# Kernel tuning notes

Measured on AMD Instinct MI355X. Metric: run time of the kernel, lower is better.

## Reference

```python
import jax, jax.numpy as jnp
import numpy as np

DIM = 1024
HEADS = 16
HEAD_DIM = DIM // HEADS
SCALE = HEAD_DIM ** -0.5


def setup_inputs() -> dict:
    key = jax.random.key(0)
    k1, k2, k3, k4 = jax.random.split(key, 4)
    x = jax.random.normal(k1, (2, 2048, DIM), dtype=jnp.float32)
    # nn.Linear(dim, 3*dim, bias=False): weight shape (3*dim, dim), y = x @ W.T
    w_qkv = jax.random.normal(k2, (3 * DIM, DIM), dtype=jnp.float32) * (DIM ** -0.5)
    w_proj = jax.random.normal(k3, (DIM, DIM), dtype=jnp.float32) * (DIM ** -0.5)
    head_w = jnp.ones((HEADS,), dtype=jnp.float32)
    return {"x": x, "w_qkv": w_qkv, "w_proj": w_proj, "head_w": head_w}


def reference(x, w_qkv, w_proj, head_w) -> jnp.ndarray:
    B, N, C = x.shape
    qkv = jnp.einsum("bnc,dc->bnd", x, w_qkv)  # [B,N,3C]
    qkv = qkv.reshape(B, N, 3, HEADS, HEAD_DIM).transpose(2, 0, 3, 1, 4)
    q, k, v = qkv[0], qkv[1], qkv[2]  # each [B,H,N,Dh]
    attn = jnp.einsum("bhqd,bhkd->bhqk", q, k) * SCALE  # [B,H,N,N]
    attn = jax.nn.softmax(attn, axis=-1)
    out = jnp.einsum("bhqk,bhkd->bhqd", attn, v)  # [B,H,N,Dh]
    hw = jax.nn.softmax(head_w)[None, :, None, None]
    out = out * hw
    out = out.transpose(0, 2, 1, 3).reshape(B, N, C)
    return jnp.einsum("bnc,dc->bnd", out, w_proj)
```

## Files before the change

### kernel.cpp

```cpp
#include <hip/hip_runtime.h>

typedef _Float16 half_t;
typedef _Float16 half8 __attribute__((ext_vector_type(8)));
typedef _Float16 half4_t __attribute__((ext_vector_type(4)));
typedef _Float16 half2_t __attribute__((ext_vector_type(2)));
typedef float floatx4 __attribute__((ext_vector_type(4)));
typedef float floatx16 __attribute__((ext_vector_type(16)));
typedef unsigned int uint4v __attribute__((ext_vector_type(4)));

#define B_SZ 2
#define SEQ 2048
#define DIM_ 1024
#define NH 16
#define DH 64
#define ROWS (B_SZ * SEQ)
#define NJS 2

__device__ __forceinline__ void gl2lds16(const void* g, void* l) {
  __builtin_amdgcn_global_load_lds((const __attribute__((address_space(1))) unsigned int*)g,
                                   (__attribute__((address_space(3))) unsigned int*)l, 16, 0, 0);
}

__device__ __forceinline__ float fexp2(float x) {
#if __has_builtin(__builtin_amdgcn_exp2f)
  return __builtin_amdgcn_exp2f(x);
#else
  return __expf(x * 0.6931471805599453f);
#endif
}

__device__ __forceinline__ unsigned cvtpk_u32(float a, float b) {
#if __has_builtin(__builtin_amdgcn_cvt_pkrtz)
  return __builtin_bit_cast(unsigned, __builtin_amdgcn_cvt_pkrtz(a, b));
#else
  half2_t h; h.x = (half_t)a; h.y = (half_t)b;
  return __builtin_bit_cast(unsigned, h);
#endif
}

__device__ __forceinline__ half8 pack8(float p0, float p1, float p2, float p3,
                                       float p4, float p5, float p6, float p7) {
  uint4v u;
  u.x = cvtpk_u32(p0, p1);
  u.y = cvtpk_u32(p2, p3);
  u.z = cvtpk_u32(p4, p5);
  u.w = cvtpk_u32(p6, p7);
  return __builtin_bit_cast(half8, u);
}

__global__ __launch_bounds__(256) void convert_all(const float4* __restrict__ x,
                                                   const float4* __restrict__ wq,
                                                   const float4* __restrict__ wp,
                                                   half4_t* __restrict__ dst,
                                                   int nx, int nq, int np) {
  int i = blockIdx.x * blockDim.x + threadIdx.x;
  float4 v;
  if (i < nx) v = x[i];
  else if (i < nx + nq) v = wq[i - nx];
  else if (i < nx + nq + np) v = wp[i - nx - nq];
  else return;
  half4_t h;
  h.x = (half_t)v.x; h.y = (half_t)v.y; h.z = (half_t)v.z; h.w = (half_t)v.w;
  dst[i] = h;
}

template <int MODE, int BN>
__global__ __launch_bounds__(256) void gemm32(const half_t* __restrict__ A,
                                              const half_t* __restrict__ Bt,
                                              half_t* __restrict__ q16,
                                              half_t* __restrict__ k16,
                                              half_t* __restrict__ vT16,
                                              float* __restrict__ outp) {
  constexpr int K = 1024;
  constexpr int NT = BN / 64;
  __shared__ __align__(16) half_t a_lds[128 * 64];
  __shared__ __align__(16) half_t b_lds[BN * 64];
  const int t = threadIdx.x;
  const int wave = t >> 6, lane = t & 63;
  const int l31 = lane & 31, hw = lane >> 5;
  const int wm = wave >> 1, wn = wave & 1;
  const int row0 = blockIdx.y * 128, col0 = blockIdx.x * BN;

  floatx16 acc[2][NT];
#pragma unroll
  for (int i = 0; i < 2; ++i)
#pragma unroll
    for (int j = 0; j < NT; ++j)
#pragma unroll
      for (int r = 0; r < 16; ++r) acc[i][j][r] = 0.f;

  for (int k0 = 0; k0 < K; k0 += 64) {
#pragma unroll
    for (int hi = 0; hi < 4; ++hi) {
      int s = t + hi * 256;
      int row = s >> 3, c = s & 7;
      int sc = c ^ (row & 7);
      gl2lds16(A + (size_t)(row0 + row) * K + (k0 + sc * 8), a_lds + (wave * 64 + hi * 256) * 8);
    }
#pragma unroll
    for (int hi = 0; hi < BN / 32; ++hi) {
      int s = t + hi * 256;
      int row = s >> 3, c = s & 7;
      int sc = c ^ (row & 7);
      gl2lds16(Bt + (size_t)(col0 + row) * K + (k0 + sc * 8), b_lds + (wave * 64 + hi * 256) * 8);
    }
    __syncthreads();
    half8 af[2][4], bf[NT][4];
#pragma unroll
    for (int mt = 0; mt < 2; ++mt) {
      int row = wm * 64 + mt * 32 + l31;
#pragma unroll
      for (int kf = 0; kf < 4; ++kf)
        af[mt][kf] = *(const half8*)(a_lds + row * 64 + ((kf * 2 + hw) ^ (row & 7)) * 8);
    }
#pragma unroll
    for (int nt = 0; nt < NT; ++nt) {
      int row = wn * (BN / 2) + nt * 32 + l31;
#pragma unroll
      for (int kf = 0; kf < 4; ++kf)
        bf[nt][kf] = *(const half8*)(b_lds + row * 64 + ((kf * 2 + hw) ^ (row & 7)) * 8);
    }
#pragma unroll
    for (int kf = 0; kf < 4; ++kf)
#pragma unroll
      for (int mt = 0; mt < 2; ++mt)
#pragma unroll
        for (int nt = 0; nt < NT; ++nt)
          acc[mt][nt] =
              __builtin_amdgcn_mfma_f32_32x32x16_f16(af[mt][kf], bf[nt][kf], acc[mt][nt], 0, 0, 0);
    __syncthreads();
  }

  if (MODE == 0) {
    const int which = col0 >> 10;
#pragma unroll
    for (int mt = 0; mt < 2; ++mt)
#pragma unroll
      for (int nt = 0; nt < NT; ++nt) {
        int growb = row0 + wm * 64 + mt * 32;
        int gcol = col0 + wn * (BN / 2) + nt * 32 + l31;
        int hc = gcol & 1023, h = hc >> 6, d = hc & 63;
        if (which == 2) {
#pragma unroll
          for (int rq = 0; rq < 4; ++rq) {
            int grow = growb + 8 * rq + 4 * hw;
            int b = grow >> 11, n0 = grow & 2047;
            int bh = b * NH + h;
            half4_t h4;
            h4.x = (half_t)acc[mt][nt][rq * 4 + 0];
            h4.y = (half_t)acc[mt][nt][rq * 4 + 1];
            h4.z = (half_t)acc[mt][nt][rq * 4 + 2];
            h4.w = (half_t)acc[mt][nt][rq * 4 + 3];
            *(half4_t*)(vT16 + ((size_t)bh * DH + d) * SEQ + n0) = h4;
          }
        } else {
#pragma unroll
          for (int r = 0; r < 16; ++r) {
            int grow = growb + (r & 3) + 8 * (r >> 2) + 4 * hw;
            int b = grow >> 11, n = grow & 2047;
            int bh = b * NH + h;
            float v = acc[mt][nt][r];
            if (which == 0)
              q16[((size_t)bh * SEQ + n) * DH + d] =
                  (half_t)(v * 0.1803368801111204f);
            else
              k16[((size_t)bh * SEQ + n) * DH + d] = (half_t)v;
          }
        }
      }
  } else {
#pragma unroll
    for (int mt = 0; mt < 2; ++mt)
#pragma unroll
      for (int nt = 0; nt < NT; ++nt) {
        int growb = row0 + wm * 64 + mt * 32;
        int gcol = col0 + wn * (BN / 2) + nt * 32 + l31;
#pragma unroll
        for (int r = 0; r < 16; ++r) {
          int grow = growb + (r & 3) + 8 * (r >> 2) + 4 * hw;
          outp[(size_t)grow * DIM_ + gcol] = acc[mt][nt][r];
        }
      }
  }
}

__global__ __launch_bounds__(256, 3) void attn_p1(const half_t* __restrict__ q16,
                                                  const half_t* __restrict__ k16,
                                                  const half_t* __restrict__ vT16,
                                                  half_t* __restrict__ opart,
                                                  float* __restrict__ psums) {
  __shared__ __align__(16) half_t k_lds[2][64 * 64];
  __shared__ __align__(16) half_t v_lds[2][64 * 64];

  const int t = threadIdx.x;
  const int wave = t >> 6, lane = t & 63;
  const int l31 = lane & 31, hw = lane >> 5;
  const int blk = blockIdx.x;
  const int js = blk & (NJS - 1), qt = (blk >> 1) & 15, bh = blk >> 5;
  const half_t* qp = q16 + (size_t)bh * SEQ * DH;
  const half_t* kp = k16 + (size_t)bh * SEQ * DH;
  const half_t* vp = vT16 + (size_t)bh * DH * SEQ;
  const int q0w = qt * 128 + wave * 32;
  const int jbase = js * (SEQ / NJS);
  constexpr int NJT = (SEQ / NJS) / 64;

  const int s0 = t, s1 = t + 256;
  const int r0_ = s0 >> 3, c0_ = (s0 & 7) ^ (r0_ & 7);
  const int r1_ = s1 >> 3, c1_ = (s1 & 7) ^ (r1_ & 7);

  half8 qf[4];
#pragma unroll
  for (int kf = 0; kf < 4; ++kf)
    qf[kf] = *(const half8*)(qp + (size_t)(q0w + l31) * DH + kf * 16 + hw * 8);

  floatx16 o[2];
#pragma unroll
  for (int i = 0; i < 2; ++i)
#pragma unroll
    for (int r = 0; r < 16; ++r) o[i][r] = 0.f;
  float psum = 0.f;

  gl2lds16(kp + (size_t)(jbase + r0_) * DH + c0_ * 8, &k_lds[0][(wave * 64) * 8]);
  gl2lds16(vp + (size_t)r0_ * SEQ + jbase + c0_ * 8, &v_lds[0][(wave * 64) * 8]);
  gl2lds16(kp + (size_t)(jbase + r1_) * DH + c1_ * 8, &k_lds[0][(wave * 64 + 256) * 8]);
  gl2lds16(vp + (size_t)r1_ * SEQ + jbase + c1_ * 8, &v_lds[0][(wave * 64 + 256) * 8]);

  int cur = 0;
  for (int jt = 0; jt < NJT; ++jt) {
    __syncthreads();

    if (jt + 1 < NJT) {
      const int j0 = jbase + (jt + 1) * 64, nb = cur ^ 1;
      gl2lds16(kp + (size_t)(j0 + r0_) * DH + c0_ * 8, &k_lds[nb][(wave * 64) * 8]);
      gl2lds16(vp + (size_t)r0_ * SEQ + j0 + c0_ * 8, &v_lds[nb][(wave * 64) * 8]);
      gl2lds16(kp + (size_t)(j0 + r1_) * DH + c1_ * 8, &k_lds[nb][(wave * 64 + 256) * 8]);
      gl2lds16(vp + (size_t)r1_ * SEQ + j0 + c1_ * 8, &v_lds[nb][(wave * 64 + 256) * 8]);
    }

    const half_t* kl = k_lds[cur];
    const half_t* vl = v_lds[cur];

    floatx16 st[2];
#pragma unroll
    for (int m = 0; m < 2; ++m)
#pragma unroll
      for (int r = 0; r < 16; ++r) st[m][r] = 0.f;
    __builtin_amdgcn_s_setprio(1);
#pragma unroll
    for (int kf = 0; kf < 4; ++kf)
#pragma unroll
      for (int m = 0; m < 2; ++m) {
        int row = m * 32 + l31;
        half8 kb = *(const half8*)(kl + row * 64 + ((kf * 2 + hw) ^ (row & 7)) * 8);
        st[m] = __builtin_amdgcn_mfma_f32_32x32x16_f16(kb, qf[kf], st[m], 0, 0, 0);
      }
    __builtin_amdgcn_s_setprio(0);

    half8 pa[2][2];
#pragma unroll
    for (int m = 0; m < 2; ++m) {
      float p[16];
#pragma unroll
      for (int r = 0; r < 16; ++r) p[r] = fexp2(st[m][r]);
      float a0 = (p[0] + p[1]) + (p[2] + p[3]);
      float a1 = (p[4] + p[5]) + (p[6] + p[7]);
      float a2 = (p[8] + p[9]) + (p[10] + p[11]);
      float a3 = (p[12] + p[13]) + (p[14] + p[15]);
      psum += (a0 + a1) + (a2 + a3);
      pa[m][0] = pack8(p[0], p[1], p[2], p[3], p[4], p[5], p[6], p[7]);
      pa[m][1] = pack8(p[8], p[9], p[10], p[11], p[12], p[13], p[14], p[15]);
    }

    __builtin_amdgcn_s_setprio(1);
#pragma unroll
    for (int s = 0; s < 4; ++s) {
#pragma unroll
      for (int dt = 0; dt < 2; ++dt) {
        int row = dt * 32 + l31;
        int ca = ((s * 2 + 0) ^ (row & 7));
        int cb = ((s * 2 + 1) ^ (row & 7));
        half4_t va = *(const half4_t*)(vl + row * 64 + ca * 8 + hw * 4);
        half4_t vb = *(const half4_t*)(vl + row * 64 + cb * 8 + hw * 4);
        half8 v8 = __builtin_shufflevector(va, vb, 0, 1, 2, 3, 4, 5, 6, 7);
        o[dt] = __builtin_amdgcn_mfma_f32_32x32x16_f16(pa[s >> 1][s & 1], v8, o[dt], 0, 0, 0);
      }
    }
    __builtin_amdgcn_s_setprio(0);
    cur ^= 1;
  }

  psum += __shfl_xor(psum, 32, 64);
  if (hw == 0) psums[((size_t)(js * 32 + bh)) * SEQ + q0w + l31] = psum;

#pragma unroll
  for (int dt = 0; dt < 2; ++dt)
#pragma unroll
    for (int r = 0; r < 16; ++r) {
      int n = q0w + (r & 3) + 8 * (r >> 2) + 4 * hw;
      opart[((size_t)(js * 32 + bh) * SEQ + n) * DH + dt * 32 + l31] = (half_t)o[dt][r];
    }
}

__global__ __launch_bounds__(256) void combine(const half_t* __restrict__ opart,
                                               const float* __restrict__ psums,
                                               const float* __restrict__ head_w,
                                               half_t* __restrict__ attn16) {
  int idx = blockIdx.x * blockDim.x + threadIdx.x;
  int d4 = idx & 15, n = (idx >> 4) & 2047, bh = idx >> 15;
  int h = bh & 15, b = bh >> 4;
  const size_t jstr = (size_t)32 * SEQ * DH;
  size_t off = ((size_t)bh * SEQ + n) * DH + d4 * 4;

  float sx = 0.f, sy = 0.f, sz = 0.f, sw2 = 0.f, ps = 0.f;
#pragma unroll
  for (int js = 0; js < NJS; ++js) {
    half4_t ov = *(const half4_t*)(opart + js * jstr + off);
    sx += (float)ov.x; sy += (float)ov.y; sz += (float)ov.z; sw2 += (float)ov.w;
    ps += psums[(size_t)js * 32 * SEQ + (size_t)bh * SEQ + n];
  }

  float mw = head_w[0];
#pragma unroll
  for (int i = 1; i < NH; ++i) mw = fmaxf(mw, head_w[i]);
  float sw = 0.f;
#pragma unroll
  for (int i = 0; i < NH; ++i) sw += __expf(head_w[i] - mw);
  float hwv = __expf(head_w[h] - mw) / sw;

  float scl = hwv / ps;
  half4_t r;
  r.x = (half_t)(sx * scl);
  r.y = (half_t)(sy * scl);
  r.z = (half_t)(sz * scl);
  r.w = (half_t)(sw2 * scl);
  *(half4_t*)(attn16 + ((size_t)(b * SEQ + n)) * DIM_ + h * DH + d4 * 4) = r;
}

extern "C" void kernel_launch(void* const* d_in, const int* in_sizes, int n_in,
                              void* d_out, int out_size, void* d_ws, size_t ws_size,
                              hipStream_t stream) {
  const float* x = (const float*)d_in[0];
  const float* w_qkv = (const float*)d_in[1];
  const float* w_proj = (const float*)d_in[2];
  const float* head_w = (const float*)d_in[3];
  float* out = (float*)d_out;

  half_t* x16 = (half_t*)d_ws;
  half_t* wq16 = x16 + (size_t)ROWS * DIM_;
  half_t* wp16 = wq16 + (size_t)3 * DIM_ * DIM_;
  half_t* q16 = wp16 + (size_t)DIM_ * DIM_;
  half_t* k16 = q16 + (size_t)ROWS * DIM_;
  half_t* vT16 = k16 + (size_t)ROWS * DIM_;
  half_t* attn16 = vT16 + (size_t)ROWS * DIM_;
  half_t* opart = attn16 + (size_t)ROWS * DIM_;
  float* psums = (float*)(opart + (size_t)NJS * 32 * SEQ * DH);

  const int nx = ROWS * DIM_ / 4, nq = 3 * DIM_ * DIM_ / 4, np = DIM_ * DIM_ / 4;
  convert_all<<<(nx + nq + np) / 256, 256, 0, stream>>>((const float4*)x, (const float4*)w_qkv,
                                                        (const float4*)w_proj, (half4_t*)x16,
                                                        nx, nq, np);

  gemm32<0, 128><<<dim3(24, 32), 256, 0, stream>>>(x16, wq16, q16, k16, vT16, nullptr);
  attn_p1<<<32 * 16 * NJS, 256, 0, stream>>>(q16, k16, vT16, opart, psums);
  combine<<<(32 * SEQ * DH / 4) / 256, 256, 0, stream>>>(opart, psums, head_w, attn16);
  gemm32<1, 64><<<dim3(16, 32), 256, 0, stream>>>(attn16, wp16, nullptr, nullptr, nullptr, out);
}
```

Measured before the change: 189.5 us.

## Use permlane32 swap to build P fragments, enabling single half8 V loads

The exp'd P values are repacked across the two half-waves with permlane32_swap, falling back to shfl_xor, so each P fragment matches a contiguous K ordering. The V operand can then be read as one swizzled half8 LDS load instead of two half4 loads plus a shuffle. The key-split factor also goes from 2 to 4, giving more blocks per head but more partial outputs for the combine step to merge. The cost is extra cross-lane ops per tile and more partial-sum traffic.

```diff
diff --git a/kernel.cpp b/kernel.cpp
--- a/kernel.cpp
+++ b/kernel.cpp
@@ -7,6 +7,7 @@
 typedef float floatx4 __attribute__((ext_vector_type(4)));
 typedef float floatx16 __attribute__((ext_vector_type(16)));
 typedef unsigned int uint4v __attribute__((ext_vector_type(4)));
+typedef unsigned int uint2v __attribute__((ext_vector_type(2)));
 
 #define B_SZ 2
 #define SEQ 2048
@@ -14,7 +15,7 @@
 #define NH 16
 #define DH 64
 #define ROWS (B_SZ * SEQ)
-#define NJS 2
+#define NJS 4
 
 __device__ __forceinline__ void gl2lds16(const void* g, void* l) {
   __builtin_amdgcn_global_load_lds((const __attribute__((address_space(1))) unsigned int*)g,
@@ -36,16 +37,6 @@
   half2_t h; h.x = (half_t)a; h.y = (half_t)b;
   return __builtin_bit_cast(unsigned, h);
 #endif
-}
-
-__device__ __forceinline__ half8 pack8(float p0, float p1, float p2, float p3,
-                                       float p4, float p5, float p6, float p7) {
-  uint4v u;
-  u.x = cvtpk_u32(p0, p1);
-  u.y = cvtpk_u32(p2, p3);
-  u.z = cvtpk_u32(p4, p5);
-  u.w = cvtpk_u32(p6, p7);
-  return __builtin_bit_cast(half8, u);
 }
 
 __global__ __launch_bounds__(256) void convert_all(const float4* __restrict__ x,
@@ -196,7 +187,7 @@
   const int wave = t >> 6, lane = t & 63;
   const int l31 = lane & 31, hw = lane >> 5;
   const int blk = blockIdx.x;
-  const int js = blk & (NJS - 1), qt = (blk >> 1) & 15, bh = blk >> 5;
+  const int js = blk & (NJS - 1), qt = (blk / NJS) & 15, bh = blk / (NJS * 16);
   const half_t* qp = q16 + (size_t)bh * SEQ * DH;
   const half_t* kp = k16 + (size_t)bh * SEQ * DH;
   const half_t* vp = vT16 + (size_t)bh * DH * SEQ;
@@ -256,35 +247,51 @@
       }
     __builtin_amdgcn_s_setprio(0);
 
-    half8 pa[2][2];
-#pragma unroll
-    for (int m = 0; m < 2; ++m) {
-      float p[16];
-#pragma unroll
-      for (int r = 0; r < 16; ++r) p[r] = fexp2(st[m][r]);
-      float a0 = (p[0] + p[1]) + (p[2] + p[3]);
-      float a1 = (p[4] + p[5]) + (p[6] + p[7]);
-      float a2 = (p[8] + p[9]) + (p[10] + p[11]);
-      float a3 = (p[12] + p[13]) + (p[14] + p[15]);
-      psum += (a0 + a1) + (a2 + a3);
-      pa[m][0] = pack8(p[0], p[1], p[2], p[3], p[4], p[5], p[6], p[7]);
-      pa[m][1] = pack8(p[8], p[9], p[10], p[11], p[12], p[13], p[14], p[15]);
+    half8 pa[4];
+#pragma unroll
+    for (int ks = 0; ks < 4; ++ks) {
+      const int m = ks >> 1, rb = (ks & 1) * 8;
+      float p0 = fexp2(st[m][rb + 0]);
+      float p1 = fexp2(st[m][rb + 1]);
+      float p2 = fexp2(st[m][rb + 2]);
+      float p3 = fexp2(st[m][rb + 3]);
+      float p4 = fexp2(st[m][rb + 4]);
+      float p5 = fexp2(st[m][rb + 5]);
+      float p6 = fexp2(st[m][rb + 6]);
+      float p7 = fexp2(st[m][rb + 7]);
+      psum += ((p0 + p1) + (p2 + p3)) + ((p4 + p5) + (p6 + p7));
+      unsigned uA = cvtpk_u32(p0, p1);
+      unsigned uB = cvtpk_u32(p2, p3);
+      unsigned uC = cvtpk_u32(p4, p5);
+      unsigned uD = cvtpk_u32(p6, p7);
+#if __has_builtin(__builtin_amdgcn_permlane32_swap)
+      uint2v sAC = __builtin_bit_cast(uint2v, __builtin_amdgcn_permlane32_swap(uA, uC, false, false));
+      uint2v sBD = __builtin_bit_cast(uint2v, __builtin_amdgcn_permlane32_swap(uB, uD, false, false));
+      uint4v u;
+      u.x = sAC.x; u.y = sBD.x; u.z = sAC.y; u.w = sBD.y;
+#else
+      unsigned xA = (unsigned)__shfl_xor((int)uA, 32, 64);
+      unsigned xB = (unsigned)__shfl_xor((int)uB, 32, 64);
+      unsigned xC = (unsigned)__shfl_xor((int)uC, 32, 64);
+      unsigned xD = (unsigned)__shfl_xor((int)uD, 32, 64);
+      uint4v u;
+      u.x = hw ? xC : uA;
+      u.y = hw ? xD : uB;
+      u.z = hw ? uC : xA;
+      u.w = hw ? uD : xB;
+#endif
+      pa[ks] = __builtin_bit_cast(half8, u);
     }
 
     __builtin_amdgcn_s_setprio(1);
 #pragma unroll
-    for (int s = 0; s < 4; ++s) {
+    for (int ks = 0; ks < 4; ++ks)
 #pragma unroll
       for (int dt = 0; dt < 2; ++dt) {
         int row = dt * 32 + l31;
-        int ca = ((s * 2 + 0) ^ (row & 7));
-        int cb = ((s * 2 + 1) ^ (row & 7));
-        half4_t va = *(const half4_t*)(vl + row * 64 + ca * 8 + hw * 4);
-        half4_t vb = *(const half4_t*)(vl + row * 64 + cb * 8 + hw * 4);
-        half8 v8 = __builtin_shufflevector(va, vb, 0, 1, 2, 3, 4, 5, 6, 7);
-        o[dt] = __builtin_amdgcn_mfma_f32_32x32x16_f16(pa[s >> 1][s & 1], v8, o[dt], 0, 0, 0);
+        half8 vb = *(const half8*)(vl + row * 64 + ((ks * 2 + hw) ^ (row & 7)) * 8);
+        o[dt] = __builtin_amdgcn_mfma_f32_32x32x16_f16(pa[ks], vb, o[dt], 0, 0, 0);
       }
-    }
     __builtin_amdgcn_s_setprio(0);
     cur ^= 1;
   }
```

Result: no change. 186.1 us (-1.8%).
